# Optimization experiments

Hardware: AMD Instinct MI355X
Metric: run time of the kernel (lower is better)

## Reference

```python
import jax, jax.numpy as jnp
import numpy as np

N_NODES = 100000
N_EDGES = 1000000
IN_FEATS = 256
OUT_FEATS = 64


def setup_inputs() -> dict:
    key = jax.random.key(0)
    k1, k2, k3, k4 = jax.random.split(key, 4)
    x = jax.random.normal(k1, (N_NODES, IN_FEATS), dtype=jnp.float32)
    src = jax.random.randint(k2, (N_EDGES,), 0, N_NODES, dtype=jnp.int64)
    dst = jax.random.randint(k3, (N_EDGES,), 0, N_NODES, dtype=jnp.int64)
    # Glorot-style init as in dgl GraphConv
    W = jax.random.normal(k4, (IN_FEATS, OUT_FEATS), dtype=jnp.float32) * (2.0 / (IN_FEATS + OUT_FEATS)) ** 0.5
    b = jnp.zeros((OUT_FEATS,), dtype=jnp.float32)
    return {"x": x, "src": src, "dst": dst, "W": W, "b": b}


def reference(x, src, dst, W, b):
    # dgl GraphConv with norm='both':
    #   h = D_in^{-1/2} * A * D_out^{-1/2} * X * W + b
    # in_feats > out_feats -> dense transform first, then sparse aggregation.
    n = x.shape[0]
    e_ones = jnp.ones(src.shape[0], dtype=x.dtype)
    deg_out = jnp.clip(jax.ops.segment_sum(e_ones, src, num_segments=n), 1.0)  # [N]
    deg_in = jnp.clip(jax.ops.segment_sum(e_ones, dst, num_segments=n), 1.0)   # [N]
    h = (x * deg_out[:, None] ** -0.5) @ W                 # [N, out]
    agg = jax.ops.segment_sum(h[src], dst, num_segments=n)  # SpMM: [N, out]
    return agg * deg_in[:, None] ** -0.5 + b
```

## Files before the change

### kernel.cpp

```cpp
#include <hip/hip_runtime.h>

#define IN_F 256
#define OUT_F 64
#define BLK1 512
#define BKT 128
#define CAP 4096

typedef __attribute__((ext_vector_type(8))) short s16x8;
typedef __attribute__((ext_vector_type(4))) float f32x4;
typedef __attribute__((ext_vector_type(4))) unsigned u32x4;

__device__ __forceinline__ unsigned short bf16_rne(float f) {
    unsigned u = __builtin_bit_cast(unsigned, f);
    u += 0x7FFFu + ((u >> 16) & 1u);
    return (unsigned short)(u >> 16);
}
__device__ __forceinline__ float bf16_lo(unsigned u) {
    return __builtin_bit_cast(float, u << 16);
}
__device__ __forceinline__ float bf16_hi(unsigned u) {
    return __builtin_bit_cast(float, u & 0xFFFF0000u);
}
__device__ __forceinline__ unsigned pk2(float a, float b) {
    unsigned r;
    asm("v_cvt_pk_bf16_f32 %0, %1, %2" : "=v"(r) : "v"(a), "v"(b));
    return r;
}

__global__ __launch_bounds__(256) void k_coarse(const int* __restrict__ src,
                                                const int* __restrict__ dst,
                                                int* __restrict__ cnt,
                                                int nb, int ne) {
    __shared__ int hD[1024], hS[1024];
    const int blk = blockIdx.x, tid = threadIdx.x;
    for (int i = tid; i < 1024; i += 256) { hD[i] = 0; hS[i] = 0; }
    __syncthreads();
    const int epb = (ne + BLK1 - 1) / BLK1;
    const int e0 = blk * epb, e1 = min(ne, e0 + epb);
    for (int e = e0 + tid; e < e1; e += 256) {
        atomicAdd(&hD[dst[e] >> 7], 1);
        atomicAdd(&hS[src[e] >> 7], 1);
    }
    __syncthreads();
    for (int bb = tid; bb < nb; bb += 256) {
        cnt[bb * BLK1 + blk] = hD[bb];
        cnt[(nb + bb) * BLK1 + blk] = hS[bb];
    }
}

__global__ __launch_bounds__(256) void k_scan1(const int* __restrict__ deg,
                                               int* __restrict__ excl,
                                               int* __restrict__ partials, int m) {
    __shared__ int sd[256];
    const int tid = threadIdx.x;
    const int idx = blockIdx.x * 1024 + tid * 4;
    int v0 = 0, v1 = 0, v2 = 0, v3 = 0;
    if (idx     < m) v0 = deg[idx];
    if (idx + 1 < m) v1 = deg[idx + 1];
    if (idx + 2 < m) v2 = deg[idx + 2];
    if (idx + 3 < m) v3 = deg[idx + 3];
    const int tsum = v0 + v1 + v2 + v3;
    sd[tid] = tsum;
    __syncthreads();
    for (int off = 1; off < 256; off <<= 1) {
        int t = (tid >= off) ? sd[tid - off] : 0;
        __syncthreads();
        sd[tid] += t;
        __syncthreads();
    }
    const int texcl = sd[tid] - tsum;
    if (tid == 255) partials[blockIdx.x] = sd[255];
    if (idx     < m) excl[idx]     = texcl;
    if (idx + 1 < m) excl[idx + 1] = texcl + v0;
    if (idx + 2 < m) excl[idx + 2] = texcl + v0 + v1;
    if (idx + 3 < m) excl[idx + 3] = texcl + v0 + v1 + v2;
}

__global__ __launch_bounds__(1024) void k_scan2(int* __restrict__ partials, int nb) {
    __shared__ int sd[1024];
    const int tid = threadIdx.x;
    const int v = (tid < nb) ? partials[tid] : 0;
    sd[tid] = v;
    __syncthreads();
    for (int off = 1; off < 1024; off <<= 1) {
        int t = (tid >= off) ? sd[tid - off] : 0;
        __syncthreads();
        sd[tid] += t;
        __syncthreads();
    }
    if (tid < nb) partials[tid] = sd[tid] - v;
}

__global__ __launch_bounds__(256) void k_part(const int* __restrict__ src,
                                              const int* __restrict__ dst,
                                              const int* __restrict__ cnt,
                                              const int* __restrict__ partials,
                                              unsigned* __restrict__ tmp,
                                              int nb, int ne) {
    __shared__ int cD[1024], cS[1024];
    const int blk = blockIdx.x, tid = threadIdx.x;
    for (int bb = tid; bb < nb; bb += 256) {
        int iD = bb * BLK1 + blk;
        int iS = (nb + bb) * BLK1 + blk;
        cD[bb] = cnt[iD] + partials[iD >> 10];
        cS[bb] = cnt[iS] + partials[iS >> 10];
    }
    __syncthreads();
    const int epb = (ne + BLK1 - 1) / BLK1;
    const int e0 = blk * epb, e1 = min(ne, e0 + epb);
    for (int e = e0 + tid; e < e1; e += 256) {
        int d = dst[e], s = src[e];
        int pD = atomicAdd(&cD[d >> 7], 1);
        tmp[pD] = ((unsigned)(d & 127) << 17) | (unsigned)s;
        int pS = atomicAdd(&cS[s >> 7], 1);
        tmp[pS] = (unsigned)(s & 127);
    }
}

__global__ __launch_bounds__(256) void k_fine_src(const int* __restrict__ cnt,
                                                  const int* __restrict__ partials,
                                                  const unsigned* __restrict__ tmp,
                                                  int* __restrict__ deg_out,
                                                  int n, int nb, int ne) {
    __shared__ int hist[BKT];
    const int b = blockIdx.x, tid = threadIdx.x;
    const int ib = (nb + b) * BLK1;
    const int base = cnt[ib] + partials[ib >> 10];
    const int ie = (nb + b + 1) * BLK1;
    const int end = (b + 1 < nb) ? (cnt[ie] + partials[ie >> 10]) : 2 * ne;
    if (tid < BKT) hist[tid] = 0;
    __syncthreads();
    for (int i = base + tid; i < end; i += 256)
        atomicAdd(&hist[tmp[i] & 127u], 1);
    __syncthreads();
    const int node = b * BKT + tid;
    if (tid < BKT && node < n) deg_out[node] = hist[tid];
}

__global__ __launch_bounds__(256, 4) void k_gemm(const float* __restrict__ x,
                                                 const float* __restrict__ W,
                                                 const int* __restrict__ deg_out,
                                                 unsigned short* __restrict__ h, int n) {
    __shared__ char lds[32768];
    const int tid = threadIdx.x;
    const int lane = tid & 63;
    const int wid = tid >> 6;

    {
        const int f = tid & 63;
        const int kg = (tid >> 6) * 64;
        const int swz = (f & 7) << 4;
#pragma unroll
        for (int j = 0; j < 16; ++j) {
            const int k0 = kg + j * 4;
            float w0 = W[(k0 + 0) * OUT_F + f];
            float w1 = W[(k0 + 1) * OUT_F + f];
            float w2 = W[(k0 + 2) * OUT_F + f];
            float w3 = W[(k0 + 3) * OUT_F + f];
            uint2 p;
            p.x = pk2(w0, w1);
            p.y = pk2(w2, w3);
            *(uint2*)(lds + f * 512 + ((k0 * 2) ^ swz)) = p;
        }
    }
    __syncthreads();

    const int r15 = lane & 15;
    const int q = lane >> 4;
    const int bswz = (r15 & 7) << 4;
    const int b_base = r15 * 512;
    const int rq = q * 4;

#pragma unroll
    for (int p = 0; p < 2; ++p) {
        const int row = blockIdx.x * 128 + p * 64 + wid * 16 + r15;
        const int rowc = min(row, n - 1);
        const float* xr = x + (size_t)rowc * IN_F + q * 8;

        f32x4 acc0 = {0.f, 0.f, 0.f, 0.f};
        f32x4 acc1 = acc0, acc2 = acc0, acc3 = acc0;

#pragma unroll
        for (int kk = 0; kk < 8; ++kk) {
            float4 a0 = *(const float4*)(xr + kk * 32);
            float4 a1 = *(const float4*)(xr + kk * 32 + 4);
            u32x4 au;
            au[0] = pk2(a0.x, a0.y);
            au[1] = pk2(a0.z, a0.w);
            au[2] = pk2(a1.x, a1.y);
            au[3] = pk2(a1.z, a1.w);
            s16x8 a = __builtin_bit_cast(s16x8, au);
            const int off = (q * 16 + kk * 64) ^ bswz;
            s16x8 b0 = *(const s16x8*)(lds + b_base + off);
            s16x8 b1 = *(const s16x8*)(lds + b_base + 8192 + off);
            s16x8 b2 = *(const s16x8*)(lds + b_base + 16384 + off);
            s16x8 b3 = *(const s16x8*)(lds + b_base + 24576 + off);
            acc0 = __builtin_amdgcn_mfma_f32_16x16x32_bf16(a, b0, acc0, 0, 0, 0);
            acc1 = __builtin_amdgcn_mfma_f32_16x16x32_bf16(a, b1, acc1, 0, 0, 0);
            acc2 = __builtin_amdgcn_mfma_f32_16x16x32_bf16(a, b2, acc2, 0, 0, 0);
            acc3 = __builtin_amdgcn_mfma_f32_16x16x32_bf16(a, b3, acc3, 0, 0, 0);
        }

#pragma unroll
        for (int j = 0; j < 4; ++j) {
            const int grow = blockIdx.x * 128 + p * 64 + wid * 16 + rq + j;
            if (grow < n) {
                const float s = rsqrtf(fmaxf((float)deg_out[grow], 1.0f));
                unsigned short* hp = h + (size_t)grow * OUT_F + r15;
                hp[0]  = bf16_rne(acc0[j] * s);
                hp[16] = bf16_rne(acc1[j] * s);
                hp[32] = bf16_rne(acc2[j] * s);
                hp[48] = bf16_rne(acc3[j] * s);
            }
        }
    }
}

__global__ __launch_bounds__(512) void k_agg(const int* __restrict__ cnt,
                                             const int* __restrict__ partials,
                                             const unsigned* __restrict__ tmp,
                                             const unsigned* __restrict__ h32,
                                             const float* __restrict__ b,
                                             float* __restrict__ out,
                                             int n, int nb, int ne) {
    __shared__ int hist[BKT], sd[BKT], cur[BKT], stt[BKT];
    __shared__ int eidx[CAP];
    const int bkt = blockIdx.x, tid = threadIdx.x;
    const int ib = bkt * BLK1;
    const int base = cnt[ib] + partials[ib >> 10];
    const int ie = (bkt + 1) * BLK1;
    const int end = (bkt + 1 < nb) ? (cnt[ie] + partials[ie >> 10]) : ne;

    if (tid < BKT) hist[tid] = 0;
    __syncthreads();
    for (int i = base + tid; i < end; i += 512)
        atomicAdd(&hist[tmp[i] >> 17], 1);
    __syncthreads();
    int dg0 = 0;
    if (tid < BKT) { dg0 = hist[tid]; sd[tid] = dg0; }
    __syncthreads();
    for (int off = 1; off < BKT; off <<= 1) {
        int t = 0;
        if (tid < BKT && tid >= off) t = sd[tid - off];
        __syncthreads();
        if (tid < BKT) sd[tid] += t;
        __syncthreads();
    }
    if (tid < BKT) {
        const int excl = sd[tid] - dg0;
        cur[tid] = excl;
        stt[tid] = excl;
    }
    __syncthreads();
    for (int i = base + tid; i < end; i += 512) {
        unsigned v = tmp[i];
        int pos = atomicAdd(&cur[v >> 17], 1);
        eidx[min(pos, CAP - 1)] = (int)(v & 0x1FFFFu);
    }
    __syncthreads();

    const int wid = tid >> 6, lane = tid & 63;
    const int f2 = lane & 31, half = lane >> 5;
    for (int nd = wid; nd < BKT; nd += 8) {
        const int node = bkt * BKT + nd;
        if (node >= n) continue;
        const int st = stt[nd];
        const int dg = hist[nd];
        float a0 = 0.f, a1 = 0.f, c0 = 0.f, c1 = 0.f;
        float d0 = 0.f, d1 = 0.f, e0 = 0.f, e1 = 0.f;
        int i = 0;
        const int dg8 = dg & ~7;
        for (; i < dg8; i += 8) {
            int s0 = eidx[st + i + half];
            int s1 = eidx[st + i + 2 + half];
            int s2 = eidx[st + i + 4 + half];
            int s3 = eidx[st + i + 6 + half];
            unsigned u0 = h32[s0 * 32 + f2];
            unsigned u1 = h32[s1 * 32 + f2];
            unsigned u2 = h32[s2 * 32 + f2];
            unsigned u3 = h32[s3 * 32 + f2];
            a0 += bf16_lo(u0); a1 += bf16_hi(u0);
            c0 += bf16_lo(u1); c1 += bf16_hi(u1);
            d0 += bf16_lo(u2); d1 += bf16_hi(u2);
            e0 += bf16_lo(u3); e1 += bf16_hi(u3);
        }
        for (; i < dg; i += 2) {
            const int e = i + half;
            const bool v = e < dg;
            int s = eidx[st + (v ? e : i)];
            unsigned u = h32[s * 32 + f2];
            if (v) { a0 += bf16_lo(u); a1 += bf16_hi(u); }
        }
        a0 += c0; a1 += c1;
        d0 += e0; d1 += e1;
        a0 += d0; a1 += d1;
        a0 += __shfl_xor(a0, 32, 64);
        a1 += __shfl_xor(a1, 32, 64);
        if (half == 0) {
            const float scale = rsqrtf(fmaxf((float)dg, 1.0f));
            float2 v;
            v.x = a0 * scale + b[f2 * 2];
            v.y = a1 * scale + b[f2 * 2 + 1];
            *(float2*)&out[(size_t)node * OUT_F + f2 * 2] = v;
        }
    }
}

extern "C" void kernel_launch(void* const* d_in, const int* in_sizes, int n_in,
                              void* d_out, int out_size, void* d_ws, size_t ws_size,
                              hipStream_t stream) {
    const float* x   = (const float*)d_in[0];
    const int*   src = (const int*)d_in[1];
    const int*   dst = (const int*)d_in[2];
    const float* W   = (const float*)d_in[3];
    const float* b   = (const float*)d_in[4];
    float* out = (float*)d_out;

    const int n  = in_sizes[0] / IN_F;
    const int ne = in_sizes[1];

    const int nb = (n + BKT - 1) / BKT;
    const int m  = 2 * nb * BLK1;

    int* cnt        = (int*)d_ws;
    int* partials   = cnt + m;
    unsigned* tmp   = (unsigned*)(partials + 1024);
    int* deg_out    = (int*)(tmp + 2 * (size_t)ne);
    unsigned short* h = (unsigned short*)(deg_out + n);

    const int nb_scan = (m + 1023) / 1024;

    k_coarse<<<BLK1, 256, 0, stream>>>(src, dst, cnt, nb, ne);
    k_scan1<<<nb_scan, 256, 0, stream>>>(cnt, cnt, partials, m);
    k_scan2<<<1, 1024, 0, stream>>>(partials, nb_scan);
    k_part<<<BLK1, 256, 0, stream>>>(src, dst, cnt, partials, tmp, nb, ne);
    k_fine_src<<<nb, 256, 0, stream>>>(cnt, partials, tmp, deg_out, n, nb, ne);
    k_gemm<<<(n + 127) / 128, 256, 0, stream>>>(x, W, deg_out, h, n);
    k_agg<<<nb, 512, 0, stream>>>(cnt, partials, tmp, (const unsigned*)h, b, out, n, nb, ne);
}
```

Before: 117.2 us.

## Shrink src partition to bytes, widen partition blocks, cache dst bucket in LDS

Doubles the number of partition blocks and their thread count, and vectorises the count scan to 8 elements per thread with int4 loads and stores, dropping bounds checks since m is now a multiple of 2048. The src-side partition entries, which only carry a 7-bit local index, are stored as bytes in a separate array instead of 32-bit words. This cuts write and read traffic in k_part and k_fine_src. k_agg loads its dst bucket once into shared memory and reuses it for the scatter pass instead of reading global memory twice, at the cost of 16KB more LDS per block, which may reduce occupancy.

```diff
diff --git a/kernel.cpp b/kernel.cpp
--- a/kernel.cpp
+++ b/kernel.cpp
@@ -2,7 +2,7 @@
 
 #define IN_F 256
 #define OUT_F 64
-#define BLK1 512
+#define BLK1 1024
 #define BKT 128
 #define CAP 4096
 
@@ -27,22 +27,22 @@
     return r;
 }
 
-__global__ __launch_bounds__(256) void k_coarse(const int* __restrict__ src,
+__global__ __launch_bounds__(512) void k_coarse(const int* __restrict__ src,
                                                 const int* __restrict__ dst,
                                                 int* __restrict__ cnt,
                                                 int nb, int ne) {
     __shared__ int hD[1024], hS[1024];
     const int blk = blockIdx.x, tid = threadIdx.x;
-    for (int i = tid; i < 1024; i += 256) { hD[i] = 0; hS[i] = 0; }
+    for (int i = tid; i < 1024; i += 512) { hD[i] = 0; hS[i] = 0; }
     __syncthreads();
     const int epb = (ne + BLK1 - 1) / BLK1;
     const int e0 = blk * epb, e1 = min(ne, e0 + epb);
-    for (int e = e0 + tid; e < e1; e += 256) {
+    for (int e = e0 + tid; e < e1; e += 512) {
         atomicAdd(&hD[dst[e] >> 7], 1);
         atomicAdd(&hS[src[e] >> 7], 1);
     }
     __syncthreads();
-    for (int bb = tid; bb < nb; bb += 256) {
+    for (int bb = tid; bb < nb; bb += 512) {
         cnt[bb * BLK1 + blk] = hD[bb];
         cnt[(nb + bb) * BLK1 + blk] = hS[bb];
     }
@@ -50,16 +50,13 @@
 
 __global__ __launch_bounds__(256) void k_scan1(const int* __restrict__ deg,
                                                int* __restrict__ excl,
-                                               int* __restrict__ partials, int m) {
+                                               int* __restrict__ partials) {
     __shared__ int sd[256];
     const int tid = threadIdx.x;
-    const int idx = blockIdx.x * 1024 + tid * 4;
-    int v0 = 0, v1 = 0, v2 = 0, v3 = 0;
-    if (idx     < m) v0 = deg[idx];
-    if (idx + 1 < m) v1 = deg[idx + 1];
-    if (idx + 2 < m) v2 = deg[idx + 2];
-    if (idx + 3 < m) v3 = deg[idx + 3];
-    const int tsum = v0 + v1 + v2 + v3;
+    const int idx = blockIdx.x * 2048 + tid * 8;
+    int4 va = *(const int4*)&deg[idx];
+    int4 vb = *(const int4*)&deg[idx + 4];
+    const int tsum = va.x + va.y + va.z + va.w + vb.x + vb.y + vb.z + vb.w;
     sd[tid] = tsum;
     __syncthreads();
     for (int off = 1; off < 256; off <<= 1) {
@@ -68,12 +65,19 @@
         sd[tid] += t;
         __syncthreads();
     }
-    const int texcl = sd[tid] - tsum;
+    int run = sd[tid] - tsum;
     if (tid == 255) partials[blockIdx.x] = sd[255];
-    if (idx     < m) excl[idx]     = texcl;
-    if (idx + 1 < m) excl[idx + 1] = texcl + v0;
-    if (idx + 2 < m) excl[idx + 2] = texcl + v0 + v1;
-    if (idx + 3 < m) excl[idx + 3] = texcl + v0 + v1 + v2;
+    int4 oa, ob;
+    oa.x = run; run += va.x;
+    oa.y = run; run += va.y;
+    oa.z = run; run += va.z;
+    oa.w = run; run += va.w;
+    ob.x = run; run += vb.x;
+    ob.y = run; run += vb.y;
+    ob.z = run; run += vb.z;
+    ob.w = run;
+    *(int4*)&excl[idx] = oa;
+    *(int4*)&excl[idx + 4] = ob;
 }
 
 __global__ __launch_bounds__(1024) void k_scan2(int* __restrict__ partials, int nb) {
@@ -91,47 +95,48 @@
     if (tid < nb) partials[tid] = sd[tid] - v;
 }
 
-__global__ __launch_bounds__(256) void k_part(const int* __restrict__ src,
+__global__ __launch_bounds__(512) void k_part(const int* __restrict__ src,
                                               const int* __restrict__ dst,
                                               const int* __restrict__ cnt,
                                               const int* __restrict__ partials,
-                                              unsigned* __restrict__ tmp,
+                                              unsigned* __restrict__ tmpD,
+                                              unsigned char* __restrict__ tmpS,
                                               int nb, int ne) {
     __shared__ int cD[1024], cS[1024];
     const int blk = blockIdx.x, tid = threadIdx.x;
-    for (int bb = tid; bb < nb; bb += 256) {
+    for (int bb = tid; bb < nb; bb += 512) {
         int iD = bb * BLK1 + blk;
         int iS = (nb + bb) * BLK1 + blk;
-        cD[bb] = cnt[iD] + partials[iD >> 10];
-        cS[bb] = cnt[iS] + partials[iS >> 10];
+        cD[bb] = cnt[iD] + partials[iD >> 11];
+        cS[bb] = cnt[iS] + partials[iS >> 11];
     }
     __syncthreads();
     const int epb = (ne + BLK1 - 1) / BLK1;
     const int e0 = blk * epb, e1 = min(ne, e0 + epb);
-    for (int e = e0 + tid; e < e1; e += 256) {
+    for (int e = e0 + tid; e < e1; e += 512) {
         int d = dst[e], s = src[e];
         int pD = atomicAdd(&cD[d >> 7], 1);
-        tmp[pD] = ((unsigned)(d & 127) << 17) | (unsigned)s;
+        tmpD[pD] = ((unsigned)(d & 127) << 17) | (unsigned)s;
         int pS = atomicAdd(&cS[s >> 7], 1);
-        tmp[pS] = (unsigned)(s & 127);
+        tmpS[pS - ne] = (unsigned char)(s & 127);
     }
 }
 
 __global__ __launch_bounds__(256) void k_fine_src(const int* __restrict__ cnt,
                                                   const int* __restrict__ partials,
-                                                  const unsigned* __restrict__ tmp,
+                                                  const unsigned char* __restrict__ tmpS,
                                                   int* __restrict__ deg_out,
                                                   int n, int nb, int ne) {
     __shared__ int hist[BKT];
     const int b = blockIdx.x, tid = threadIdx.x;
     const int ib = (nb + b) * BLK1;
-    const int base = cnt[ib] + partials[ib >> 10];
+    const int base = cnt[ib] + partials[ib >> 11] - ne;
     const int ie = (nb + b + 1) * BLK1;
-    const int end = (b + 1 < nb) ? (cnt[ie] + partials[ie >> 10]) : 2 * ne;
+    const int end = (b + 1 < nb) ? (cnt[ie] + partials[ie >> 11] - ne) : ne;
     if (tid < BKT) hist[tid] = 0;
     __syncthreads();
     for (int i = base + tid; i < end; i += 256)
-        atomicAdd(&hist[tmp[i] & 127u], 1);
+        atomicAdd(&hist[tmpS[i] & 127u], 1);
     __syncthreads();
     const int node = b * BKT + tid;
     if (tid < BKT && node < n) deg_out[node] = hist[tid];
@@ -218,23 +223,28 @@
 
 __global__ __launch_bounds__(512) void k_agg(const int* __restrict__ cnt,
                                              const int* __restrict__ partials,
-                                             const unsigned* __restrict__ tmp,
+                                             const unsigned* __restrict__ tmpD,
                                              const unsigned* __restrict__ h32,
                                              const float* __restrict__ b,
                                              float* __restrict__ out,
                                              int n, int nb, int ne) {
     __shared__ int hist[BKT], sd[BKT], cur[BKT], stt[BKT];
+    __shared__ unsigned raw[CAP];
     __shared__ int eidx[CAP];
     const int bkt = blockIdx.x, tid = threadIdx.x;
     const int ib = bkt * BLK1;
-    const int base = cnt[ib] + partials[ib >> 10];
+    const int base = cnt[ib] + partials[ib >> 11];
     const int ie = (bkt + 1) * BLK1;
-    const int end = (bkt + 1 < nb) ? (cnt[ie] + partials[ie >> 10]) : ne;
+    const int end = (bkt + 1 < nb) ? (cnt[ie] + partials[ie >> 11]) : ne;
+    const int cnt_e = min(end - base, CAP);
 
     if (tid < BKT) hist[tid] = 0;
     __syncthreads();
-    for (int i = base + tid; i < end; i += 512)
-        atomicAdd(&hist[tmp[i] >> 17], 1);
+    for (int i = tid; i < cnt_e; i += 512) {
+        unsigned v = tmpD[base + i];
+        raw[i] = v;
+        atomicAdd(&hist[v >> 17], 1);
+    }
     __syncthreads();
     int dg0 = 0;
     if (tid < BKT) { dg0 = hist[tid]; sd[tid] = dg0; }
@@ -252,8 +262,8 @@
         stt[tid] = excl;
     }
     __syncthreads();
-    for (int i = base + tid; i < end; i += 512) {
-        unsigned v = tmp[i];
+    for (int i = tid; i < cnt_e; i += 512) {
+        unsigned v = raw[i];
         int pos = atomicAdd(&cur[v >> 17], 1);
         eidx[min(pos, CAP - 1)] = (int)(v & 0x1FFFFu);
     }
@@ -322,19 +332,20 @@
     const int nb = (n + BKT - 1) / BKT;
     const int m  = 2 * nb * BLK1;
 
-    int* cnt        = (int*)d_ws;
-    int* partials   = cnt + m;
-    unsigned* tmp   = (unsigned*)(partials + 1024);
-    int* deg_out    = (int*)(tmp + 2 * (size_t)ne);
+    int* cnt          = (int*)d_ws;
+    int* partials     = cnt + m;
+    unsigned* tmpD    = (unsigned*)(partials + 1024);
+    unsigned char* tmpS = (unsigned char*)(tmpD + ne);
+    int* deg_out      = (int*)(tmpS + ((ne + 15) & ~15));
     unsigned short* h = (unsigned short*)(deg_out + n);
 
-    const int nb_scan = (m + 1023) / 1024;
-
-    k_coarse<<<BLK1, 256, 0, stream>>>(src, dst, cnt, nb, ne);
-    k_scan1<<<nb_scan, 256, 0, stream>>>(cnt, cnt, partials, m);
+    const int nb_scan = m / 2048;
+
+    k_coarse<<<BLK1, 512, 0, stream>>>(src, dst, cnt, nb, ne);
+    k_scan1<<<nb_scan, 256, 0, stream>>>(cnt, cnt, partials);
     k_scan2<<<1, 1024, 0, stream>>>(partials, nb_scan);
-    k_part<<<BLK1, 256, 0, stream>>>(src, dst, cnt, partials, tmp, nb, ne);
-    k_fine_src<<<nb, 256, 0, stream>>>(cnt, partials, tmp, deg_out, n, nb, ne);
+    k_part<<<BLK1, 512, 0, stream>>>(src, dst, cnt, partials, tmpD, tmpS, nb, ne);
+    k_fine_src<<<nb, 256, 0, stream>>>(cnt, partials, tmpS, deg_out, n, nb, ne);
     k_gemm<<<(n + 127) / 128, 256, 0, stream>>>(x, W, deg_out, h, n);
-    k_agg<<<nb, 512, 0, stream>>>(cnt, partials, tmp, (const unsigned*)h, b, out, n, nb, ne);
-}
+    k_agg<<<nb, 512, 0, stream>>>(cnt, partials, tmpD, (const unsigned*)h, b, out, n, nb, ne);
+}
```

New measurement: 117.4 us. About the same (+0.2%).
